# Kernel optimization log

Hardware: AMD Instinct MI355X
Metric: run time of the kernel (lower is better)

The kernel has to match this reference:

```python
import jax, jax.numpy as jnp
import numpy as np
from jax import lax

EPS = 1e-6

def _ln(x):
    # LayerNorm32 over channel dim, computed in fp32
    x32 = x.astype(jnp.float32)
    mu = jnp.mean(x32, axis=-1, keepdims=True)
    var = jnp.mean(jnp.square(x32 - mu), axis=-1, keepdims=True)
    return ((x32 - mu) * lax.rsqrt(var + EPS)).astype(x.dtype)

def _downsample2(f, mask):
    # mean over active voxels in each 2x2x2 cell; f must already be zero at inactive voxels
    B, D, H, W, C = f.shape
    fs = f.reshape(B, D // 2, 2, H // 2, 2, W // 2, 2, C).sum(axis=(2, 4, 6))
    cnt = mask.reshape(B, D // 2, 2, H // 2, 2, W // 2, 2).astype(f.dtype).sum(axis=(2, 4, 6))
    out = fs / jnp.maximum(cnt, 1.0)[..., None]
    return out, cnt > 0

def _subm_conv3(x, w, b, mask_f):
    # submanifold sparse conv == dense SAME conv on zero-filled grid, masked to active set
    y = lax.conv_general_dilated(x, w, window_strides=(1, 1, 1), padding='SAME',
                                 dimension_numbers=('NDHWC', 'DHWIO', 'NDHWC'))
    return (y + b) * mask_f


def setup_inputs() -> dict:
    key = jax.random.key(0)
    ks = jax.random.split(key, 6)
    B, D, C, CO = 4, 64, 64, 128
    feats = jax.random.normal(ks[0], (B, D, D, D, C), jnp.float32)
    mask = jax.random.uniform(ks[1], (B, D, D, D)) < 0.3
    gamma1 = jnp.ones((C,), jnp.float32)
    beta1 = jnp.zeros((C,), jnp.float32)
    w1 = jax.random.normal(ks[2], (3, 3, 3, C, CO), jnp.float32) / np.sqrt(27.0 * C)
    b1 = jnp.zeros((CO,), jnp.float32)
    # conv2 is zero-initialized in the original (zero_module); we use small random
    # weights so the reference is numerically non-degenerate
    w2 = jax.random.normal(ks[3], (3, 3, 3, CO, CO), jnp.float32) / np.sqrt(27.0 * CO)
    b2 = jnp.zeros((CO,), jnp.float32)
    w_skip = jax.random.normal(ks[4], (C, CO), jnp.float32) / np.sqrt(C)
    b_skip = jnp.zeros((CO,), jnp.float32)
    return dict(feats=feats, mask=mask, gamma1=gamma1, beta1=beta1,
                w1=w1, b1=b1, w2=w2, b2=b2, w_skip=w_skip, b_skip=b_skip)


def reference(feats, mask, gamma1, beta1, w1, b1, w2, b2, w_skip, b_skip):
    m = mask[..., None].astype(feats.dtype)          # [B,D,H,W,1]
    h = (_ln(feats) * gamma1 + beta1)                # norm1 (affine)
    h = jax.nn.silu(h) * m                           # silu, restrict to active set
    xm = feats * m
    h, mask2 = _downsample2(h, mask)                 # SparseDownsample(2) on h
    x_ds, _ = _downsample2(xm, mask)                 # SparseDownsample(2) on x
    m2 = mask2[..., None].astype(feats.dtype)
    h = _subm_conv3(h, w1, b1, m2)                   # conv1
    h = jax.nn.silu(_ln(h)) * m2                     # norm2 (no affine) + silu
    h = _subm_conv3(h, w2, b2, m2)                   # conv2
    skip = (x_ds @ w_skip + b_skip) * m2             # SparseLinear skip
    return h + skip
```

## Files before the change

### kernel.cpp

```cpp
#include <hip/hip_runtime.h>
#include <hip/hip_bf16.h>

#define EPS 1e-6f
typedef unsigned short b16;
typedef __attribute__((ext_vector_type(8))) short v8s;
typedef __attribute__((ext_vector_type(4))) float v4f;

typedef const __attribute__((address_space(1))) void* gptr_t;
typedef __attribute__((address_space(3))) void* lptr_t;

__device__ __forceinline__ b16 f2b(float f) {
    __hip_bfloat16 h = __float2bfloat16(f);
    return *reinterpret_cast<b16*>(&h);
}
__device__ __forceinline__ float siluf(float x){ return x / (1.f + __expf(-x)); }

__device__ __forceinline__ void gll16(const b16* g, b16* l) {
    __builtin_amdgcn_global_load_lds((gptr_t)g, (lptr_t)l, 16, 0, 0);
}

template<int IC>
__global__ void __launch_bounds__(256) k_wt(const float* __restrict__ w, b16* __restrict__ o, int tot) {
    int i = blockIdx.x*256 + threadIdx.x;
    if (i >= tot) return;
    int ic = i % IC; int oc = (i / IC) & 127; int tap = i / (IC*128);
    o[i] = f2b(w[(tap*IC + ic)*128 + oc]);
}

template<int IC>
__global__ void __launch_bounds__(256) k_wtb(const float* __restrict__ w, b16* __restrict__ o, int tot) {
    int i = blockIdx.x*256 + threadIdx.x;
    if (i >= tot) return;
    constexpr int ICB = IC/32;
    int icl = i & 31;
    int oc  = (i >> 5) & 127;
    int r   = i >> 12;
    int tap = r / ICB, icb = r % ICB;
    o[i] = f2b(w[(tap*IC + icb*32 + icl)*128 + oc]);
}

__global__ void __launch_bounds__(256) k_ln_down(
    const float* __restrict__ feats, const int* __restrict__ mask,
    const float* __restrict__ gamma, const float* __restrict__ beta,
    b16* __restrict__ h_ds_pad, b16* __restrict__ x_ds, float* __restrict__ cnt_out)
{
    int wave = (blockIdx.x * 256 + threadIdx.x) >> 6;
    int lane = threadIdx.x & 63;
    int x = wave & 31, y = (wave >> 5) & 31, z = (wave >> 10) & 31, b = wave >> 15;
    float g = gamma[lane], be = beta[lane];
    float hacc = 0.f, xacc = 0.f, cnt = 0.f;
    #pragma unroll
    for (int i = 0; i < 8; ++i) {
        int zz = 2*z + (i>>2), yy = 2*y + ((i>>1)&1), xx = 2*x + (i&1);
        int vox = ((b*64 + zz)*64 + yy)*64 + xx;
        int m = mask[vox];
        float val = feats[vox*64 + lane];
        float s1 = val, s2 = val*val;
        #pragma unroll
        for (int off = 32; off > 0; off >>= 1) {
            s1 += __shfl_xor(s1, off, 64);
            s2 += __shfl_xor(s2, off, 64);
        }
        float mu = s1 * (1.f/64.f);
        float var = fmaxf(s2 * (1.f/64.f) - mu*mu, 0.f);
        float h = (val - mu) * rsqrtf(var + EPS) * g + be;
        h = siluf(h);
        if (m != 0) { hacc += h; xacc += val; cnt += 1.f; }
    }
    float inv = 1.f / fmaxf(cnt, 1.f);
    long vp = ((long)(b*34 + z+1)*34 + (y+1))*34 + (x+1);
    h_ds_pad[vp*64 + lane] = f2b(hacc * inv);
    x_ds[(long)wave*64 + lane] = f2b(xacc * inv);
    if (lane == 0) cnt_out[wave] = cnt;
}

template<int IC, bool IS_CONV1>
__global__ void __launch_bounds__(256) k_conv_mfma(
    const b16* __restrict__ inp,
    const b16* __restrict__ wt,
    const float* __restrict__ bias,
    const float* __restrict__ cnt,
    const b16* __restrict__ x_ds,
    const b16* __restrict__ wst,
    const float* __restrict__ b_skip,
    b16* __restrict__ h2out,
    float* __restrict__ out)
{
    constexpr int ICB = IC/32;
    constexpr int NK = 27*ICB;
    __shared__ b16 lA[2][4096];
    __shared__ b16 lB[2][4096];

    int bid = blockIdx.x;
    int y0 = (bid & 7) << 2;
    int z  = (bid >> 3) & 31;
    int b  = bid >> 8;
    int t  = threadIdx.x;
    int lane = t & 63;
    int w = t >> 6;
    int col = lane & 15;
    int quad = lane >> 4;

    const b16* gAsrc[2];
    const b16* gBsrc[2];
    {
        int vsub = lane >> 2;
        int s    = lane & 3;
        #pragma unroll
        for (int j = 0; j < 2; ++j) {
            int x  = j*16 + vsub;
            int cA = (s - (x >> 1)) & 3;
            gAsrc[j] = inp + ((long)((b*34 + z)*34 + (y0 + w))*34 + x)*IC + cA*8;
            int oc = w*32 + j*16 + vsub;
            int cB = (s - (vsub >> 1)) & 3;
            gBsrc[j] = wt + oc*32 + cB*8;
        }
    }

    int so   = ((quad + (col>>1)) & 3) * 8;
    int aoff = w*1024 + col*32 + so;
    int boff = col*32 + so;

    v4f acc[2][8];
    #pragma unroll
    for (int tl=0;tl<2;++tl)
        #pragma unroll
        for (int n=0;n<8;++n) acc[tl][n] = (v4f){0.f,0.f,0.f,0.f};

    long offAn = 0;
    int icbn = 0, kxn = 0, kyn = 0;
    auto advance = [&]() {
        ++icbn; offAn += 32;
        if (icbn == ICB) {
            icbn = 0;
            ++kxn;
            if (kxn == 3) {
                kxn = 0; ++kyn;
                if (kyn == 3) { kyn = 0; offAn += (long)(34*34 - 2*34 - 3)*IC; }
                else          {           offAn += (long)(34 - 3)*IC; }
            }
        }
    };

    auto stage = [&](long offA, long offB, int buf) {
        #pragma unroll
        for (int j = 0; j < 2; ++j) {
            gll16(gAsrc[j] + offA, &lA[buf][w*1024 + j*512]);
            gll16(gBsrc[j] + offB, &lB[buf][w*1024 + j*512]);
        }
    };

    stage(0, 0, 0);
    advance();
    long offBn = 4096;
    __syncthreads();

    int cur = 0;
    for (int k = 0; k < NK; ++k) {
        if (k + 1 < NK) {
            stage(offAn, offBn, cur ^ 1);
            advance();
            offBn += 4096;
        }
        v8s a0 = *(const v8s*)(&lA[cur][aoff]);
        v8s a1 = *(const v8s*)(&lA[cur][aoff + 512]);
        __builtin_amdgcn_s_setprio(1);
        #pragma unroll
        for (int n = 0; n < 8; ++n) {
            v8s bb = *(const v8s*)(&lB[cur][n*512 + boff]);
            acc[0][n] = __builtin_amdgcn_mfma_f32_16x16x32_bf16(a0, bb, acc[0][n], 0,0,0);
            acc[1][n] = __builtin_amdgcn_mfma_f32_16x16x32_bf16(a1, bb, acc[1][n], 0,0,0);
        }
        __builtin_amdgcn_s_setprio(0);
        __syncthreads();
        cur ^= 1;
    }

    int yrow = y0 + w;
    long cellrow = ((long)(b*32+z)*32 + yrow)*32;

    if (!IS_CONV1) {
        const b16* X0 = x_ds + (cellrow + col)*64 + quad*8;
        const b16* X1 = X0 + 16*64;
        const b16* WS = wst + col*64 + quad*8;
        #pragma unroll
        for (int s = 0; s < 2; ++s) {
            v8s a0 = *(const v8s*)(X0 + s*32);
            v8s a1 = *(const v8s*)(X1 + s*32);
            #pragma unroll
            for (int n=0;n<8;++n) {
                v8s bb = *(const v8s*)(WS + n*16*64 + s*32);
                acc[0][n] = __builtin_amdgcn_mfma_f32_16x16x32_bf16(a0, bb, acc[0][n], 0,0,0);
                acc[1][n] = __builtin_amdgcn_mfma_f32_16x16x32_bf16(a1, bb, acc[1][n], 0,0,0);
            }
        }
    }

    float bv[8];
    #pragma unroll
    for (int n=0;n<8;++n)
        bv[n] = bias[n*16+col] + (IS_CONV1 ? 0.f : b_skip[n*16+col]);

    long prow = ((long)(b*34 + z+1)*34 + (yrow+1))*34 + 1;

    #pragma unroll
    for (int tl=0; tl<2; ++tl) {
        if (IS_CONV1) {
            float s1[4], s2[4];
            #pragma unroll
            for (int r=0;r<4;++r){
                float a=0.f, q=0.f;
                #pragma unroll
                for (int n=0;n<8;++n){ float v = acc[tl][n][r] + bv[n]; a+=v; q+=v*v; }
                s1[r]=a; s2[r]=q;
            }
            #pragma unroll
            for (int off=1; off<16; off<<=1){
                #pragma unroll
                for (int r=0;r<4;++r){ s1[r]+=__shfl_xor(s1[r],off); s2[r]+=__shfl_xor(s2[r],off); }
            }
            #pragma unroll
            for (int r=0;r<4;++r){
                int row = quad*4 + r;
                int x = tl*16 + row;
                float c = cnt[cellrow + x];
                float mu = s1[r]*(1.f/128.f);
                float var = fmaxf(s2[r]*(1.f/128.f) - mu*mu, 0.f);
                float rs = rsqrtf(var + EPS);
                bool act = c > 0.f;
                #pragma unroll
                for (int n=0;n<8;++n){
                    float v = acc[tl][n][r] + bv[n];
                    float hv = act ? siluf((v-mu)*rs) : 0.f;
                    h2out[(prow + x)*128 + n*16 + col] = f2b(hv);
                }
            }
        } else {
            #pragma unroll
            for (int r=0;r<4;++r){
                int row = quad*4 + r;
                int x = tl*16 + row;
                float c = cnt[cellrow + x];
                bool act = c > 0.f;
                #pragma unroll
                for (int n=0;n<8;++n){
                    float v = acc[tl][n][r] + bv[n];
                    out[(cellrow + x)*128 + n*16 + col] = act ? v : 0.f;
                }
            }
        }
    }
}

extern "C" void kernel_launch(void* const* d_in, const int* in_sizes, int n_in,
                              void* d_out, int out_size, void* d_ws, size_t ws_size,
                              hipStream_t stream) {
    const float* feats  = (const float*)d_in[0];
    const int*   mask   = (const int*)  d_in[1];
    const float* gamma1 = (const float*)d_in[2];
    const float* beta1  = (const float*)d_in[3];
    const float* w1     = (const float*)d_in[4];
    const float* b1     = (const float*)d_in[5];
    const float* w2     = (const float*)d_in[6];
    const float* b2     = (const float*)d_in[7];
    const float* w_skip = (const float*)d_in[8];
    const float* b_skip = (const float*)d_in[9];
    float* out = (float*)d_out;

    char* ws = (char*)d_ws;
    b16*   h_ds_pad = (b16*)(ws);
    b16*   h2_pad   = (b16*)(ws + 20123648);
    b16*   x_ds     = (b16*)(ws + 60370944);
    float* cnt      = (float*)(ws + 77148160);
    b16*   w1t      = (b16*)(ws + 77672448);
    b16*   w2t      = (b16*)(ws + 78114816);
    b16*   wst      = (b16*)(ws + 78999552);

    hipMemsetAsync(h_ds_pad, 0, 20123648, stream);
    hipMemsetAsync(h2_pad,   0, 40247296, stream);

    const int n_w1 = 27*64*128;
    const int n_w2 = 27*128*128;
    const int n_ws = 64*128;
    k_wtb<64> <<<(n_w1 + 255)/256, 256, 0, stream>>>(w1, w1t, n_w1);
    k_wtb<128><<<(n_w2 + 255)/256, 256, 0, stream>>>(w2, w2t, n_w2);
    k_wt<64>  <<<(n_ws + 255)/256, 256, 0, stream>>>(w_skip, wst, n_ws);

    k_ln_down<<<32768, 256, 0, stream>>>(feats, mask, gamma1, beta1, h_ds_pad, x_ds, cnt);

    k_conv_mfma<64,true><<<1024, 256, 0, stream>>>(h_ds_pad, w1t, b1, cnt,
                                                   nullptr, nullptr, nullptr,
                                                   h2_pad, nullptr);
    k_conv_mfma<128,false><<<1024, 256, 0, stream>>>(h2_pad, w2t, b2, cnt,
                                                     x_ds, wst, b_skip,
                                                     nullptr, out);
}
```

Measured before the change: 734.0 us.

## Use DPP reductions in LayerNorm, swizzle conv block order, set occupancy hints

Replaces the shuffle-based 64-lane reductions in the LayerNorm/downsample kernel with DPP row operations plus a swizzle and one cross-half shuffle, to cut LDS-routed shuffle traffic. The conv kernels get a remapped block index that interleaves blocks across spatial tiles, which may help L2 locality or balance across XCDs. The s_setprio calls around the MFMA loop are removed, and __launch_bounds__(256,4) wrappers ask for at least four blocks per CU, which could raise register pressure or cause spills.

```diff
diff --git a/kernel.cpp b/kernel.cpp
--- a/kernel.cpp
+++ b/kernel.cpp
@@ -17,6 +17,21 @@
 
 __device__ __forceinline__ void gll16(const b16* g, b16* l) {
     __builtin_amdgcn_global_load_lds((gptr_t)g, (lptr_t)l, 16, 0, 0);
+}
+
+__device__ __forceinline__ float red64(float s) {
+    int t;
+    t = __builtin_amdgcn_update_dpp(0, __float_as_int(s), 0x121, 0xF, 0xF, false);
+    s += __int_as_float(t);
+    t = __builtin_amdgcn_update_dpp(0, __float_as_int(s), 0x122, 0xF, 0xF, false);
+    s += __int_as_float(t);
+    t = __builtin_amdgcn_update_dpp(0, __float_as_int(s), 0x124, 0xF, 0xF, false);
+    s += __int_as_float(t);
+    t = __builtin_amdgcn_update_dpp(0, __float_as_int(s), 0x128, 0xF, 0xF, false);
+    s += __int_as_float(t);
+    s += __int_as_float(__builtin_amdgcn_ds_swizzle(__float_as_int(s), 0x401F));
+    s += __shfl_xor(s, 32, 64);
+    return s;
 }
 
 template<int IC>
@@ -55,12 +70,8 @@
         int vox = ((b*64 + zz)*64 + yy)*64 + xx;
         int m = mask[vox];
         float val = feats[vox*64 + lane];
-        float s1 = val, s2 = val*val;
-        #pragma unroll
-        for (int off = 32; off > 0; off >>= 1) {
-            s1 += __shfl_xor(s1, off, 64);
-            s2 += __shfl_xor(s2, off, 64);
-        }
+        float s1 = red64(val);
+        float s2 = red64(val*val);
         float mu = s1 * (1.f/64.f);
         float var = fmaxf(s2 * (1.f/64.f) - mu*mu, 0.f);
         float h = (val - mu) * rsqrtf(var + EPS) * g + be;
@@ -75,7 +86,7 @@
 }
 
 template<int IC, bool IS_CONV1>
-__global__ void __launch_bounds__(256) k_conv_mfma(
+__device__ __forceinline__ void conv_body(
     const b16* __restrict__ inp,
     const b16* __restrict__ wt,
     const float* __restrict__ bias,
@@ -91,7 +102,7 @@
     __shared__ b16 lA[2][4096];
     __shared__ b16 lB[2][4096];
 
-    int bid = blockIdx.x;
+    int bid = ((blockIdx.x & 7) << 7) | (blockIdx.x >> 3);
     int y0 = (bid & 7) << 2;
     int z  = (bid >> 3) & 31;
     int b  = bid >> 8;
@@ -164,14 +175,12 @@
         }
         v8s a0 = *(const v8s*)(&lA[cur][aoff]);
         v8s a1 = *(const v8s*)(&lA[cur][aoff + 512]);
-        __builtin_amdgcn_s_setprio(1);
         #pragma unroll
         for (int n = 0; n < 8; ++n) {
             v8s bb = *(const v8s*)(&lB[cur][n*512 + boff]);
             acc[0][n] = __builtin_amdgcn_mfma_f32_16x16x32_bf16(a0, bb, acc[0][n], 0,0,0);
             acc[1][n] = __builtin_amdgcn_mfma_f32_16x16x32_bf16(a1, bb, acc[1][n], 0,0,0);
         }
-        __builtin_amdgcn_s_setprio(0);
         __syncthreads();
         cur ^= 1;
     }
@@ -252,6 +261,23 @@
     }
 }
 
+__global__ void __launch_bounds__(256, 4) k_conv1(
+    const b16* __restrict__ inp, const b16* __restrict__ wt,
+    const float* __restrict__ bias, const float* __restrict__ cnt,
+    b16* __restrict__ h2out)
+{
+    conv_body<64, true>(inp, wt, bias, cnt, nullptr, nullptr, nullptr, h2out, nullptr);
+}
+
+__global__ void __launch_bounds__(256, 4) k_conv2(
+    const b16* __restrict__ inp, const b16* __restrict__ wt,
+    const float* __restrict__ bias, const float* __restrict__ cnt,
+    const b16* __restrict__ x_ds, const b16* __restrict__ wst,
+    const float* __restrict__ b_skip, float* __restrict__ out)
+{
+    conv_body<128, false>(inp, wt, bias, cnt, x_ds, wst, b_skip, nullptr, out);
+}
+
 extern "C" void kernel_launch(void* const* d_in, const int* in_sizes, int n_in,
                               void* d_out, int out_size, void* d_ws, size_t ws_size,
                               hipStream_t stream) {
@@ -288,10 +314,6 @@
 
     k_ln_down<<<32768, 256, 0, stream>>>(feats, mask, gamma1, beta1, h_ds_pad, x_ds, cnt);
 
-    k_conv_mfma<64,true><<<1024, 256, 0, stream>>>(h_ds_pad, w1t, b1, cnt,
-                                                   nullptr, nullptr, nullptr,
-                                                   h2_pad, nullptr);
-    k_conv_mfma<128,false><<<1024, 256, 0, stream>>>(h2_pad, w2t, b2, cnt,
-                                                     x_ds, wst, b_skip,
-                                                     nullptr, out);
-}
+    k_conv1<<<1024, 256, 0, stream>>>(h_ds_pad, w1t, b1, cnt, h2_pad);
+    k_conv2<<<1024, 256, 0, stream>>>(h2_pad, w2t, b2, cnt, x_ds, wst, b_skip, out);
+}
```

New measurement: 621.8 us. 15.3% less time.
